# Optimization experiments

Measured on AMD Instinct MI355X. Metric: run time of the kernel, lower is better.

The kernel has to match this reference:

```python
import jax, jax.numpy as jnp
import numpy as np

N_NODES = 50000
N_EDGES = 800000
IN_FEATS = 512
NUM_HEADS = 4
OUT_FEATS = 64
NEG_SLOPE = 0.2


def setup_inputs() -> dict:
    key = jax.random.key(0)
    k1, k2, k3, k4, k5, k6 = jax.random.split(key, 6)
    feat = jax.random.normal(k1, (N_NODES, IN_FEATS), dtype=jnp.float32)
    W = jax.random.normal(k2, (IN_FEATS, NUM_HEADS * OUT_FEATS), dtype=jnp.float32) * (1.0 / np.sqrt(IN_FEATS))
    attn_l = jax.random.normal(k3, (NUM_HEADS, OUT_FEATS), dtype=jnp.float32) * (1.0 / np.sqrt(OUT_FEATS))
    attn_r = jax.random.normal(k4, (NUM_HEADS, OUT_FEATS), dtype=jnp.float32) * (1.0 / np.sqrt(OUT_FEATS))
    src = jax.random.randint(k5, (N_EDGES,), 0, N_NODES, dtype=jnp.int32)
    dst = jax.random.randint(k6, (N_EDGES,), 0, N_NODES, dtype=jnp.int32)
    return {"feat": feat, "W": W, "attn_l": attn_l, "attn_r": attn_r, "src": src, "dst": dst}


def reference(feat, W, attn_l, attn_r, src, dst):
    N = feat.shape[0]
    H, D = attn_l.shape
    # node-wise projection: fc(feat).view(N, H, D)
    ft = (feat @ W).reshape(N, H, D)
    # per-node attention logits
    el = jnp.einsum('nhd,hd->nh', ft, attn_l)  # [N, H]
    er = jnp.einsum('nhd,hd->nh', ft, attn_r)  # [N, H]
    # edge-wise score: leaky_relu(el[u] + er[v])
    e = jax.nn.leaky_relu(el[src] + er[dst], negative_slope=NEG_SLOPE)  # [E, H]
    # segment softmax over incoming edges of each destination node
    e_max = jax.ops.segment_max(e, dst, num_segments=N)  # [N, H]
    e_max = jnp.where(jnp.isfinite(e_max), e_max, 0.0)
    exp_e = jnp.exp(e - e_max[dst])  # [E, H]
    denom = jax.ops.segment_sum(exp_e, dst, num_segments=N)  # [N, H]
    a = exp_e / denom[dst]  # [E, H]
    # weighted message aggregation: sum_u a(u,v) * ft[u]
    msg = ft[src] * a[:, :, None]  # [E, H, D]
    out = jax.ops.segment_sum(msg, dst, num_segments=N)  # [N, H, D]
    return out.reshape(N, H * D)
```

## Files before the change

### kernel.cpp

```cpp
#include <hip/hip_runtime.h>

#define N_NODES 50000
#define N_EDGES 800000
#define IN_F    512
#define NH      4
#define DH      64
#define HD      256
#define NEG     0.2f
#define NB      ((N_NODES + 255) / 256)

typedef __attribute__((ext_vector_type(8))) short bf16x8;
typedef __attribute__((ext_vector_type(4))) float f32x4;

__device__ __forceinline__ unsigned short f2bf(float x) {
    unsigned u = __float_as_uint(x);
    unsigned r = (u + 0x7FFFu + ((u >> 16) & 1u)) >> 16;
    return (unsigned short)r;
}
__device__ __forceinline__ float bf2f(unsigned short b) {
    return __uint_as_float((unsigned)b << 16);
}

__global__ __launch_bounds__(256) void setup_kernel(const float* __restrict__ W,
                                                    unsigned short* __restrict__ Wtb,
                                                    int* __restrict__ counts) {
    int b = blockIdx.x;
    if (b < NB) {
        int i = b * 256 + threadIdx.x;
        if (i < N_NODES) counts[i] = 0;
    } else {
        int i = (b - NB) * 256 + threadIdx.x;
        if (i < IN_F * HD) {
            int k = i >> 8;
            int n = i & 255;
            Wtb[(size_t)n * IN_F + k] = f2bf(W[i]);
        }
    }
}

__global__ __launch_bounds__(256) void count_kernel(const int* __restrict__ dst,
                                                    int* __restrict__ counts) {
    int e = blockIdx.x * blockDim.x + threadIdx.x;
    if (e < N_EDGES) atomicAdd(&counts[dst[e]], 1);
}

#define LDPA 72
#define LDPB 72
__global__ __launch_bounds__(256) void gemm_kernel(const float* __restrict__ A,
                                                   const unsigned short* __restrict__ Wtb,
                                                   const float* __restrict__ attn_l,
                                                   const float* __restrict__ attn_r,
                                                   unsigned short* __restrict__ Cb,
                                                   float* __restrict__ el,
                                                   float* __restrict__ er) {
    __shared__ short A_s[64][LDPA];
    __shared__ short B_s[256][LDPB];

    const int tid  = threadIdx.x;
    const int lane = tid & 63;
    const int w    = tid >> 6;
    const int lm   = lane & 15;
    const int quad = lane >> 4;
    const int row0 = blockIdx.x * 64;

    const int srow = tid >> 3;
    const int sc8  = (tid & 7) * 8;

    f32x4 acc[4][4] = {};
    float4 pa[4];
    bf16x8 pb[8];

#define LOAD_TILES(KT)                                                         \
    {                                                                          \
        int g0 = row0 + srow;                                                  \
        if (g0 < N_NODES) {                                                    \
            const float* ap = A + (size_t)g0 * IN_F + (KT) + sc8;              \
            pa[0] = *(const float4*)ap; pa[1] = *(const float4*)(ap + 4);      \
        } else { pa[0] = pa[1] = make_float4(0.f, 0.f, 0.f, 0.f); }            \
        int g1 = row0 + 32 + srow;                                             \
        if (g1 < N_NODES) {                                                    \
            const float* ap = A + (size_t)g1 * IN_F + (KT) + sc8;              \
            pa[2] = *(const float4*)ap; pa[3] = *(const float4*)(ap + 4);      \
        } else { pa[2] = pa[3] = make_float4(0.f, 0.f, 0.f, 0.f); }            \
        _Pragma("unroll")                                                      \
        for (int it = 0; it < 8; it++) {                                       \
            int brow = it * 32 + srow;                                         \
            pb[it] = *(const bf16x8*)(Wtb + (size_t)brow * IN_F +              \
                                      (KT) + sc8);                             \
        }                                                                      \
    }

    LOAD_TILES(0);

    for (int kt = 0; kt < IN_F; kt += 64) {
        {
            bf16x8 s;
            s[0] = (short)f2bf(pa[0].x); s[1] = (short)f2bf(pa[0].y);
            s[2] = (short)f2bf(pa[0].z); s[3] = (short)f2bf(pa[0].w);
            s[4] = (short)f2bf(pa[1].x); s[5] = (short)f2bf(pa[1].y);
            s[6] = (short)f2bf(pa[1].z); s[7] = (short)f2bf(pa[1].w);
            *(bf16x8*)(&A_s[srow][sc8]) = s;
            s[0] = (short)f2bf(pa[2].x); s[1] = (short)f2bf(pa[2].y);
            s[2] = (short)f2bf(pa[2].z); s[3] = (short)f2bf(pa[2].w);
            s[4] = (short)f2bf(pa[3].x); s[5] = (short)f2bf(pa[3].y);
            s[6] = (short)f2bf(pa[3].z); s[7] = (short)f2bf(pa[3].w);
            *(bf16x8*)(&A_s[32 + srow][sc8]) = s;
#pragma unroll
            for (int it = 0; it < 8; it++)
                *(bf16x8*)(&B_s[it * 32 + srow][sc8]) = pb[it];
        }
        __syncthreads();

        if (kt + 64 < IN_F) LOAD_TILES(kt + 64);

#pragma unroll
        for (int kk = 0; kk < 64; kk += 32) {
            bf16x8 af[4], bfr[4];
#pragma unroll
            for (int i = 0; i < 4; i++)
                af[i] = *(const bf16x8*)(&A_s[i * 16 + lm][kk + quad * 8]);
#pragma unroll
            for (int j = 0; j < 4; j++)
                bfr[j] = *(const bf16x8*)(&B_s[w * 64 + j * 16 + lm][kk + quad * 8]);
#pragma unroll
            for (int i = 0; i < 4; i++)
#pragma unroll
                for (int j = 0; j < 4; j++)
                    acc[i][j] = __builtin_amdgcn_mfma_f32_16x16x32_bf16(
                        af[i], bfr[j], acc[i][j], 0, 0, 0);
        }
        __syncthreads();
    }
#undef LOAD_TILES

#pragma unroll
    for (int i = 0; i < 4; i++) {
#pragma unroll
        for (int j = 0; j < 4; j++) {
            int gcol = w * 64 + j * 16 + lm;
#pragma unroll
            for (int r = 0; r < 4; r++) {
                int grow = row0 + i * 16 + quad * 4 + r;
                if (grow < N_NODES)
                    Cb[(size_t)grow * HD + gcol] = f2bf(acc[i][j][r]);
            }
        }
    }

    {
        float al[4], ar[4];
#pragma unroll
        for (int j = 0; j < 4; j++) {
            al[j] = attn_l[w * DH + j * 16 + lm];
            ar[j] = attn_r[w * DH + j * 16 + lm];
        }
#pragma unroll
        for (int i = 0; i < 4; i++) {
#pragma unroll
            for (int r = 0; r < 4; r++) {
                float sl = 0.f, sr = 0.f;
#pragma unroll
                for (int j = 0; j < 4; j++) {
                    sl += acc[i][j][r] * al[j];
                    sr += acc[i][j][r] * ar[j];
                }
#pragma unroll
                for (int off = 8; off > 0; off >>= 1) {
                    sl += __shfl_xor(sl, off);
                    sr += __shfl_xor(sr, off);
                }
                if (lm == 0) {
                    int grow = row0 + i * 16 + quad * 4 + r;
                    if (grow < N_NODES) {
                        el[(size_t)grow * NH + w] = sl;
                        er[(size_t)grow * NH + w] = sr;
                    }
                }
            }
        }
    }
}

__global__ __launch_bounds__(256) void partial_kernel(const int* __restrict__ counts,
                                                      int* __restrict__ bsums) {
    __shared__ int red[4];
    int i = blockIdx.x * 256 + threadIdx.x;
    int c = (i < N_NODES) ? counts[i] : 0;
#pragma unroll
    for (int off = 32; off > 0; off >>= 1) c += __shfl_down(c, off);
    if ((threadIdx.x & 63) == 0) red[threadIdx.x >> 6] = c;
    __syncthreads();
    if (threadIdx.x == 0) bsums[blockIdx.x] = red[0] + red[1] + red[2] + red[3];
}

__global__ __launch_bounds__(256) void bscan_kernel(const int* __restrict__ bsums,
                                                    int* __restrict__ boffs) {
    __shared__ int s[256];
    int tid = threadIdx.x;
    s[tid] = (tid < NB) ? bsums[tid] : 0;
    __syncthreads();
    for (int off = 1; off < 256; off <<= 1) {
        int x = s[tid];
        int a = (tid >= off) ? s[tid - off] : 0;
        __syncthreads();
        s[tid] = x + a;
        __syncthreads();
    }
    if (tid < NB) boffs[tid] = (tid > 0) ? s[tid - 1] : 0;
}

__global__ __launch_bounds__(256) void scatter_scan_kernel(const int* __restrict__ counts,
                                                           const int* __restrict__ boffs,
                                                           int* __restrict__ offsets,
                                                           int* __restrict__ cursor) {
    __shared__ int s[256];
    int tid = threadIdx.x;
    int i = blockIdx.x * 256 + tid;
    s[tid] = (i < N_NODES) ? counts[i] : 0;
    __syncthreads();
    for (int off = 1; off < 256; off <<= 1) {
        int x = s[tid];
        int a = (tid >= off) ? s[tid - off] : 0;
        __syncthreads();
        s[tid] = x + a;
        __syncthreads();
    }
    int excl = (tid > 0) ? s[tid - 1] : 0;
    int o = boffs[blockIdx.x] + excl;
    if (i < N_NODES) { offsets[i] = o; cursor[i] = o; }
    if (i == 0) offsets[N_NODES] = N_EDGES;
}

__device__ __forceinline__ float lrelu_exp(float x) {
    float y = (x > 0.f) ? x : NEG * x;
    return __expf(y);
}

__global__ __launch_bounds__(256) void edge_place_kernel(const int* __restrict__ src,
                                                         const int* __restrict__ dst,
                                                         const float* __restrict__ el,
                                                         const float* __restrict__ er,
                                                         int* __restrict__ cursor,
                                                         int* __restrict__ srcs,
                                                         float* __restrict__ w4s) {
    int e = blockIdx.x * blockDim.x + threadIdx.x;
    if (e >= N_EDGES) return;
    int u = src[e], v = dst[e];
    float4 l = *(const float4*)(el + (size_t)u * NH);
    float4 r = *(const float4*)(er + (size_t)v * NH);
    float4 s;
    s.x = lrelu_exp(l.x + r.x);
    s.y = lrelu_exp(l.y + r.y);
    s.z = lrelu_exp(l.z + r.z);
    s.w = lrelu_exp(l.w + r.w);
    int pos = atomicAdd(&cursor[v], 1);
    srcs[pos] = u;
    *(float4*)(w4s + (size_t)pos * NH) = s;
}

__global__ __launch_bounds__(256) void agg_kernel(const unsigned short* __restrict__ ftb,
                                                  const float* __restrict__ w4s,
                                                  const int* __restrict__ srcs,
                                                  const int* __restrict__ offsets,
                                                  float* __restrict__ out) {
    int wv   = (blockIdx.x * blockDim.x + threadIdx.x) >> 6;
    int lane = threadIdx.x & 63;
    if (wv >= N_NODES) return;

    const int beg = offsets[wv];
    const int end = offsets[wv + 1];
    const int h   = lane >> 4;
    const size_t foff = (size_t)lane * 4;

    float4 acc = make_float4(0.f, 0.f, 0.f, 0.f);
    float dsum = 0.f;

    const int n4 = (end - beg) >> 2;
    int u0, u1, u2, u3;
    if (n4 > 0) {
        const int* sp = srcs + beg;
        u0 = sp[0]; u1 = sp[1]; u2 = sp[2]; u3 = sp[3];
        for (int b = 0; b < n4; b++) {
            const int base = beg + b * 4;
            int v0 = 0, v1 = 0, v2 = 0, v3 = 0;
            if (b + 1 < n4) {
                const int* np = srcs + base + 4;
                v0 = np[0]; v1 = np[1]; v2 = np[2]; v3 = np[3];
            }
            ushort4 f0 = *(const ushort4*)(ftb + (size_t)u0 * HD + foff);
            ushort4 f1 = *(const ushort4*)(ftb + (size_t)u1 * HD + foff);
            ushort4 f2 = *(const ushort4*)(ftb + (size_t)u2 * HD + foff);
            ushort4 f3 = *(const ushort4*)(ftb + (size_t)u3 * HD + foff);
            float w0 = w4s[(size_t)(base + 0) * NH + h];
            float w1 = w4s[(size_t)(base + 1) * NH + h];
            float w2 = w4s[(size_t)(base + 2) * NH + h];
            float w3 = w4s[(size_t)(base + 3) * NH + h];
            acc.x += w0 * bf2f(f0.x) + w1 * bf2f(f1.x) + w2 * bf2f(f2.x) + w3 * bf2f(f3.x);
            acc.y += w0 * bf2f(f0.y) + w1 * bf2f(f1.y) + w2 * bf2f(f2.y) + w3 * bf2f(f3.y);
            acc.z += w0 * bf2f(f0.z) + w1 * bf2f(f1.z) + w2 * bf2f(f2.z) + w3 * bf2f(f3.z);
            acc.w += w0 * bf2f(f0.w) + w1 * bf2f(f1.w) + w2 * bf2f(f2.w) + w3 * bf2f(f3.w);
            dsum += (w0 + w1) + (w2 + w3);
            u0 = v0; u1 = v1; u2 = v2; u3 = v3;
        }
    }
    for (int p = beg + n4 * 4; p < end; p++) {
        int u = srcs[p];
        float w = w4s[(size_t)p * NH + h];
        ushort4 f = *(const ushort4*)(ftb + (size_t)u * HD + foff);
        acc.x += w * bf2f(f.x);
        acc.y += w * bf2f(f.y);
        acc.z += w * bf2f(f.z);
        acc.w += w * bf2f(f.w);
        dsum += w;
    }

    float inv = (dsum > 0.f) ? (1.f / dsum) : 0.f;
    acc.x *= inv; acc.y *= inv; acc.z *= inv; acc.w *= inv;
    *(float4*)(out + (size_t)wv * HD + foff) = acc;
}

extern "C" void kernel_launch(void* const* d_in, const int* in_sizes, int n_in,
                              void* d_out, int out_size, void* d_ws, size_t ws_size,
                              hipStream_t stream) {
    const float* feat   = (const float*)d_in[0];
    const float* W      = (const float*)d_in[1];
    const float* attn_l = (const float*)d_in[2];
    const float* attn_r = (const float*)d_in[3];
    const int*   src    = (const int*)d_in[4];
    const int*   dst    = (const int*)d_in[5];
    float* out = (float*)d_out;

    char* p = (char*)d_ws;
    auto alloc = [&](size_t bytes) -> char* {
        char* r = p;
        p += (bytes + 255) & ~(size_t)255;
        return r;
    };
    unsigned short* ftb     = (unsigned short*)alloc((size_t)N_NODES * HD * 2);
    unsigned short* Wtb     = (unsigned short*)alloc((size_t)IN_F * HD * 2);
    float*          el      = (float*)alloc((size_t)N_NODES * NH * 4);
    float*          er      = (float*)alloc((size_t)N_NODES * NH * 4);
    float*          w4s     = (float*)alloc((size_t)N_EDGES * NH * 4);
    int*            srcs    = (int*)alloc((size_t)N_EDGES * 4);
    int*            counts  = (int*)alloc((size_t)N_NODES * 4);
    int*            offsets = (int*)alloc((size_t)(N_NODES + 1) * 4);
    int*            cursor  = (int*)alloc((size_t)N_NODES * 4);
    int*            bsums   = (int*)alloc((size_t)NB * 4);
    int*            boffs   = (int*)alloc((size_t)NB * 4);

    setup_kernel<<<NB + (IN_F * HD + 255) / 256, 256, 0, stream>>>(W, Wtb, counts);
    count_kernel<<<(N_EDGES + 255) / 256, 256, 0, stream>>>(dst, counts);
    gemm_kernel<<<(N_NODES + 63) / 64, 256, 0, stream>>>(feat, Wtb, attn_l, attn_r,
                                                         ftb, el, er);
    partial_kernel<<<NB, 256, 0, stream>>>(counts, bsums);
    bscan_kernel<<<1, 256, 0, stream>>>(bsums, boffs);
    scatter_scan_kernel<<<NB, 256, 0, stream>>>(counts, boffs, offsets, cursor);
    edge_place_kernel<<<(N_EDGES + 255) / 256, 256, 0, stream>>>(src, dst, el, er,
                                                                 cursor, srcs, w4s);
    agg_kernel<<<(N_NODES + 3) / 4, 256, 0, stream>>>(ftb, w4s, srcs, offsets, out);
}
```

Before: 345.0 us.

## Fuse edge weights into aggregation, stage W via direct-to-LDS double-buffered loads

Edge attention weights are no longer computed and written in edge_place_kernel. agg_kernel now recomputes leaky_relu+exp from el[src] and er[dst], which removes the w4s buffer (write plus read of 12.8MB). The aggregation loop is unrolled to 8 edges, with a masked branchless tail. The GEMM pre-swizzles W into tiled XOR-permuted blocks and streams them with global_load_lds into a double-buffered LDS tile, dropping register staging for B. In exchange, LDS use goes up to 64KB for B, and el is gathered redundantly per edge.

Result: no change. 345.6 us (+0.2%).

```diff
diff --git a/kernel.cpp b/kernel.cpp
--- a/kernel.cpp
+++ b/kernel.cpp
@@ -22,7 +22,7 @@
 }
 
 __global__ __launch_bounds__(256) void setup_kernel(const float* __restrict__ W,
-                                                    unsigned short* __restrict__ Wtb,
+                                                    unsigned short* __restrict__ WtbT,
                                                     int* __restrict__ counts) {
     int b = blockIdx.x;
     if (b < NB) {
@@ -33,7 +33,12 @@
         if (i < IN_F * HD) {
             int k = i >> 8;
             int n = i & 255;
-            Wtb[(size_t)n * IN_F + k] = f2bf(W[i]);
+            int t  = k >> 6;
+            int kk = k & 63;
+            int g  = kk >> 3;
+            int w8 = kk & 7;
+            int p  = n * 8 + (g ^ (n & 7));
+            WtbT[(size_t)t * 16384 + p * 8 + w8] = f2bf(W[i]);
         }
     }
 }
@@ -45,16 +50,15 @@
 }
 
 #define LDPA 72
-#define LDPB 72
 __global__ __launch_bounds__(256) void gemm_kernel(const float* __restrict__ A,
-                                                   const unsigned short* __restrict__ Wtb,
+                                                   const unsigned short* __restrict__ WtbT,
                                                    const float* __restrict__ attn_l,
                                                    const float* __restrict__ attn_r,
                                                    unsigned short* __restrict__ Cb,
                                                    float* __restrict__ el,
                                                    float* __restrict__ er) {
     __shared__ short A_s[64][LDPA];
-    __shared__ short B_s[256][LDPB];
+    __shared__ short B_s[2][256 * 64];
 
     const int tid  = threadIdx.x;
     const int lane = tid & 63;
@@ -68,9 +72,20 @@
 
     f32x4 acc[4][4] = {};
     float4 pa[4];
-    bf16x8 pb[8];
-
-#define LOAD_TILES(KT)                                                         \
+
+#define STAGE_B(BUF, T)                                                         \
+    {                                                                           \
+        const char* gsrc = (const char*)WtbT + (size_t)(T) * 32768 + tid * 16;  \
+        char* ldst = (char*)&B_s[BUF][0] + tid * 16;                            \
+        _Pragma("unroll")                                                       \
+        for (int r = 0; r < 8; r++)                                             \
+            __builtin_amdgcn_global_load_lds(                                   \
+                (const __attribute__((address_space(1))) unsigned int*)(gsrc + r * 4096), \
+                (__attribute__((address_space(3))) unsigned int*)(ldst + r * 4096),       \
+                16, 0, 0);                                                      \
+    }
+
+#define LOAD_A(KT)                                                             \
     {                                                                          \
         int g0 = row0 + srow;                                                  \
         if (g0 < N_NODES) {                                                    \
@@ -82,17 +97,13 @@
             const float* ap = A + (size_t)g1 * IN_F + (KT) + sc8;              \
             pa[2] = *(const float4*)ap; pa[3] = *(const float4*)(ap + 4);      \
         } else { pa[2] = pa[3] = make_float4(0.f, 0.f, 0.f, 0.f); }            \
-        _Pragma("unroll")                                                      \
-        for (int it = 0; it < 8; it++) {                                       \
-            int brow = it * 32 + srow;                                         \
-            pb[it] = *(const bf16x8*)(Wtb + (size_t)brow * IN_F +              \
-                                      (KT) + sc8);                             \
-        }                                                                      \
-    }
-
-    LOAD_TILES(0);
-
-    for (int kt = 0; kt < IN_F; kt += 64) {
+    }
+
+    STAGE_B(0, 0);
+    LOAD_A(0);
+
+    int buf = 0;
+    for (int t = 0; t < 8; t++) {
         {
             bf16x8 s;
             s[0] = (short)f2bf(pa[0].x); s[1] = (short)f2bf(pa[0].y);
@@ -105,13 +116,10 @@
             s[4] = (short)f2bf(pa[3].x); s[5] = (short)f2bf(pa[3].y);
             s[6] = (short)f2bf(pa[3].z); s[7] = (short)f2bf(pa[3].w);
             *(bf16x8*)(&A_s[32 + srow][sc8]) = s;
-#pragma unroll
-            for (int it = 0; it < 8; it++)
-                *(bf16x8*)(&B_s[it * 32 + srow][sc8]) = pb[it];
         }
         __syncthreads();
 
-        if (kt + 64 < IN_F) LOAD_TILES(kt + 64);
+        if (t + 1 < 8) { STAGE_B(buf ^ 1, t + 1); LOAD_A((t + 1) * 64); }
 
 #pragma unroll
         for (int kk = 0; kk < 64; kk += 32) {
@@ -120,8 +128,12 @@
             for (int i = 0; i < 4; i++)
                 af[i] = *(const bf16x8*)(&A_s[i * 16 + lm][kk + quad * 8]);
 #pragma unroll
-            for (int j = 0; j < 4; j++)
-                bfr[j] = *(const bf16x8*)(&B_s[w * 64 + j * 16 + lm][kk + quad * 8]);
+            for (int j = 0; j < 4; j++) {
+                int n  = w * 64 + j * 16 + lm;
+                int g  = (kk >> 3) + quad;
+                int gs = g ^ (lm & 7);
+                bfr[j] = *(const bf16x8*)(&B_s[buf][(n * 8 + gs) * 8]);
+            }
 #pragma unroll
             for (int i = 0; i < 4; i++)
 #pragma unroll
@@ -129,9 +141,11 @@
                     acc[i][j] = __builtin_amdgcn_mfma_f32_16x16x32_bf16(
                         af[i], bfr[j], acc[i][j], 0, 0, 0);
         }
-        __syncthreads();
-    }
-#undef LOAD_TILES
+        if (t < 7) __syncthreads();
+        buf ^= 1;
+    }
+#undef LOAD_A
+#undef STAGE_B
 
 #pragma unroll
     for (int i = 0; i < 4; i++) {
@@ -231,35 +245,25 @@
     if (i == 0) offsets[N_NODES] = N_EDGES;
 }
 
-__device__ __forceinline__ float lrelu_exp(float x) {
-    float y = (x > 0.f) ? x : NEG * x;
-    return __expf(y);
-}
-
 __global__ __launch_bounds__(256) void edge_place_kernel(const int* __restrict__ src,
                                                          const int* __restrict__ dst,
-                                                         const float* __restrict__ el,
-                                                         const float* __restrict__ er,
                                                          int* __restrict__ cursor,
-                                                         int* __restrict__ srcs,
-                                                         float* __restrict__ w4s) {
+                                                         int* __restrict__ srcs) {
     int e = blockIdx.x * blockDim.x + threadIdx.x;
     if (e >= N_EDGES) return;
     int u = src[e], v = dst[e];
-    float4 l = *(const float4*)(el + (size_t)u * NH);
-    float4 r = *(const float4*)(er + (size_t)v * NH);
-    float4 s;
-    s.x = lrelu_exp(l.x + r.x);
-    s.y = lrelu_exp(l.y + r.y);
-    s.z = lrelu_exp(l.z + r.z);
-    s.w = lrelu_exp(l.w + r.w);
     int pos = atomicAdd(&cursor[v], 1);
     srcs[pos] = u;
-    *(float4*)(w4s + (size_t)pos * NH) = s;
+}
+
+__device__ __forceinline__ float lrelu_exp(float x) {
+    float y = fmaxf(x, NEG * x);
+    return __expf(y);
 }
 
 __global__ __launch_bounds__(256) void agg_kernel(const unsigned short* __restrict__ ftb,
-                                                  const float* __restrict__ w4s,
+                                                  const float* __restrict__ el,
+                                                  const float* __restrict__ er,
                                                   const int* __restrict__ srcs,
                                                   const int* __restrict__ offsets,
                                                   float* __restrict__ out) {
@@ -271,47 +275,101 @@
     const int end = offsets[wv + 1];
     const int h   = lane >> 4;
     const size_t foff = (size_t)lane * 4;
+    const float erv = er[(size_t)wv * NH + h];
 
     float4 acc = make_float4(0.f, 0.f, 0.f, 0.f);
     float dsum = 0.f;
 
-    const int n4 = (end - beg) >> 2;
-    int u0, u1, u2, u3;
-    if (n4 > 0) {
+    const int n8 = (end - beg) >> 3;
+    int u0, u1, u2, u3, u4, u5, u6, u7;
+    if (n8 > 0) {
         const int* sp = srcs + beg;
         u0 = sp[0]; u1 = sp[1]; u2 = sp[2]; u3 = sp[3];
-        for (int b = 0; b < n4; b++) {
-            const int base = beg + b * 4;
-            int v0 = 0, v1 = 0, v2 = 0, v3 = 0;
-            if (b + 1 < n4) {
-                const int* np = srcs + base + 4;
+        u4 = sp[4]; u5 = sp[5]; u6 = sp[6]; u7 = sp[7];
+        for (int b = 0; b < n8; b++) {
+            const int base = beg + b * 8;
+            int v0 = 0, v1 = 0, v2 = 0, v3 = 0, v4 = 0, v5 = 0, v6 = 0, v7 = 0;
+            if (b + 1 < n8) {
+                const int* np = srcs + base + 8;
                 v0 = np[0]; v1 = np[1]; v2 = np[2]; v3 = np[3];
+                v4 = np[4]; v5 = np[5]; v6 = np[6]; v7 = np[7];
             }
             ushort4 f0 = *(const ushort4*)(ftb + (size_t)u0 * HD + foff);
             ushort4 f1 = *(const ushort4*)(ftb + (size_t)u1 * HD + foff);
             ushort4 f2 = *(const ushort4*)(ftb + (size_t)u2 * HD + foff);
             ushort4 f3 = *(const ushort4*)(ftb + (size_t)u3 * HD + foff);
-            float w0 = w4s[(size_t)(base + 0) * NH + h];
-            float w1 = w4s[(size_t)(base + 1) * NH + h];
-            float w2 = w4s[(size_t)(base + 2) * NH + h];
-            float w3 = w4s[(size_t)(base + 3) * NH + h];
-            acc.x += w0 * bf2f(f0.x) + w1 * bf2f(f1.x) + w2 * bf2f(f2.x) + w3 * bf2f(f3.x);
-            acc.y += w0 * bf2f(f0.y) + w1 * bf2f(f1.y) + w2 * bf2f(f2.y) + w3 * bf2f(f3.y);
-            acc.z += w0 * bf2f(f0.z) + w1 * bf2f(f1.z) + w2 * bf2f(f2.z) + w3 * bf2f(f3.z);
-            acc.w += w0 * bf2f(f0.w) + w1 * bf2f(f1.w) + w2 * bf2f(f2.w) + w3 * bf2f(f3.w);
-            dsum += (w0 + w1) + (w2 + w3);
+            ushort4 f4 = *(const ushort4*)(ftb + (size_t)u4 * HD + foff);
+            ushort4 f5 = *(const ushort4*)(ftb + (size_t)u5 * HD + foff);
+            ushort4 f6 = *(const ushort4*)(ftb + (size_t)u6 * HD + foff);
+            ushort4 f7 = *(const ushort4*)(ftb + (size_t)u7 * HD + foff);
+            float e0 = el[(size_t)u0 * NH + h];
+            float e1 = el[(size_t)u1 * NH + h];
+            float e2 = el[(size_t)u2 * NH + h];
+            float e3 = el[(size_t)u3 * NH + h];
+            float e4 = el[(size_t)u4 * NH + h];
+            float e5 = el[(size_t)u5 * NH + h];
+            float e6 = el[(size_t)u6 * NH + h];
+            float e7 = el[(size_t)u7 * NH + h];
+            float w0 = lrelu_exp(e0 + erv), w1 = lrelu_exp(e1 + erv);
+            float w2 = lrelu_exp(e2 + erv), w3 = lrelu_exp(e3 + erv);
+            float w4 = lrelu_exp(e4 + erv), w5 = lrelu_exp(e5 + erv);
+            float w6 = lrelu_exp(e6 + erv), w7 = lrelu_exp(e7 + erv);
+            acc.x += w0 * bf2f(f0.x) + w1 * bf2f(f1.x) + w2 * bf2f(f2.x) + w3 * bf2f(f3.x)
+                   + w4 * bf2f(f4.x) + w5 * bf2f(f5.x) + w6 * bf2f(f6.x) + w7 * bf2f(f7.x);
+            acc.y += w0 * bf2f(f0.y) + w1 * bf2f(f1.y) + w2 * bf2f(f2.y) + w3 * bf2f(f3.y)
+                   + w4 * bf2f(f4.y) + w5 * bf2f(f5.y) + w6 * bf2f(f6.y) + w7 * bf2f(f7.y);
+            acc.z += w0 * bf2f(f0.z) + w1 * bf2f(f1.z) + w2 * bf2f(f2.z) + w3 * bf2f(f3.z)
+                   + w4 * bf2f(f4.z) + w5 * bf2f(f5.z) + w6 * bf2f(f6.z) + w7 * bf2f(f7.z);
+            acc.w += w0 * bf2f(f0.w) + w1 * bf2f(f1.w) + w2 * bf2f(f2.w) + w3 * bf2f(f3.w)
+                   + w4 * bf2f(f4.w) + w5 * bf2f(f5.w) + w6 * bf2f(f6.w) + w7 * bf2f(f7.w);
+            dsum += ((w0 + w1) + (w2 + w3)) + ((w4 + w5) + (w6 + w7));
             u0 = v0; u1 = v1; u2 = v2; u3 = v3;
-        }
-    }
-    for (int p = beg + n4 * 4; p < end; p++) {
-        int u = srcs[p];
-        float w = w4s[(size_t)p * NH + h];
-        ushort4 f = *(const ushort4*)(ftb + (size_t)u * HD + foff);
-        acc.x += w * bf2f(f.x);
-        acc.y += w * bf2f(f.y);
-        acc.z += w * bf2f(f.z);
-        acc.w += w * bf2f(f.w);
-        dsum += w;
+            u4 = v4; u5 = v5; u6 = v6; u7 = v7;
+        }
+    }
+    {
+        const int p0  = beg + n8 * 8;
+        const int rem = end - p0;
+        if (rem > 0) {
+            const int* sp = srcs + p0;
+            int x0 = sp[0];
+            int x1 = (1 < rem) ? sp[1] : x0;
+            int x2 = (2 < rem) ? sp[2] : x0;
+            int x3 = (3 < rem) ? sp[3] : x0;
+            int x4 = (4 < rem) ? sp[4] : x0;
+            int x5 = (5 < rem) ? sp[5] : x0;
+            int x6 = (6 < rem) ? sp[6] : x0;
+            ushort4 f0 = *(const ushort4*)(ftb + (size_t)x0 * HD + foff);
+            ushort4 f1 = *(const ushort4*)(ftb + (size_t)x1 * HD + foff);
+            ushort4 f2 = *(const ushort4*)(ftb + (size_t)x2 * HD + foff);
+            ushort4 f3 = *(const ushort4*)(ftb + (size_t)x3 * HD + foff);
+            ushort4 f4 = *(const ushort4*)(ftb + (size_t)x4 * HD + foff);
+            ushort4 f5 = *(const ushort4*)(ftb + (size_t)x5 * HD + foff);
+            ushort4 f6 = *(const ushort4*)(ftb + (size_t)x6 * HD + foff);
+            float e0 = el[(size_t)x0 * NH + h];
+            float e1 = el[(size_t)x1 * NH + h];
+            float e2 = el[(size_t)x2 * NH + h];
+            float e3 = el[(size_t)x3 * NH + h];
+            float e4 = el[(size_t)x4 * NH + h];
+            float e5 = el[(size_t)x5 * NH + h];
+            float e6 = el[(size_t)x6 * NH + h];
+            float w0 = lrelu_exp(e0 + erv);
+            float w1 = (1 < rem) ? lrelu_exp(e1 + erv) : 0.f;
+            float w2 = (2 < rem) ? lrelu_exp(e2 + erv) : 0.f;
+            float w3 = (3 < rem) ? lrelu_exp(e3 + erv) : 0.f;
+            float w4 = (4 < rem) ? lrelu_exp(e4 + erv) : 0.f;
+            float w5 = (5 < rem) ? lrelu_exp(e5 + erv) : 0.f;
+            float w6 = (6 < rem) ? lrelu_exp(e6 + erv) : 0.f;
+            acc.x += w0 * bf2f(f0.x) + w1 * bf2f(f1.x) + w2 * bf2f(f2.x) + w3 * bf2f(f3.x)
+                   + w4 * bf2f(f4.x) + w5 * bf2f(f5.x) + w6 * bf2f(f6.x);
+            acc.y += w0 * bf2f(f0.y) + w1 * bf2f(f1.y) + w2 * bf2f(f2.y) + w3 * bf2f(f3.y)
+                   + w4 * bf2f(f4.y) + w5 * bf2f(f5.y) + w6 * bf2f(f6.y);
+            acc.z += w0 * bf2f(f0.z) + w1 * bf2f(f1.z) + w2 * bf2f(f2.z) + w3 * bf2f(f3.z)
+                   + w4 * bf2f(f4.z) + w5 * bf2f(f5.z) + w6 * bf2f(f6.z);
+            acc.w += w0 * bf2f(f0.w) + w1 * bf2f(f1.w) + w2 * bf2f(f2.w) + w3 * bf2f(f3.w)
+                   + w4 * bf2f(f4.w) + w5 * bf2f(f5.w) + w6 * bf2f(f6.w);
+            dsum += ((w0 + w1) + (w2 + w3)) + ((w4 + w5) + w6);
+        }
     }
 
     float inv = (dsum > 0.f) ? (1.f / dsum) : 0.f;
@@ -337,10 +395,9 @@
         return r;
     };
     unsigned short* ftb     = (unsigned short*)alloc((size_t)N_NODES * HD * 2);
-    unsigned short* Wtb     = (unsigned short*)alloc((size_t)IN_F * HD * 2);
+    unsigned short* WtbT    = (unsigned short*)alloc((size_t)IN_F * HD * 2);
     float*          el      = (float*)alloc((size_t)N_NODES * NH * 4);
     float*          er      = (float*)alloc((size_t)N_NODES * NH * 4);
-    float*          w4s     = (float*)alloc((size_t)N_EDGES * NH * 4);
     int*            srcs    = (int*)alloc((size_t)N_EDGES * 4);
     int*            counts  = (int*)alloc((size_t)N_NODES * 4);
     int*            offsets = (int*)alloc((size_t)(N_NODES + 1) * 4);
@@ -348,14 +405,13 @@
     int*            bsums   = (int*)alloc((size_t)NB * 4);
     int*            boffs   = (int*)alloc((size_t)NB * 4);
 
-    setup_kernel<<<NB + (IN_F * HD + 255) / 256, 256, 0, stream>>>(W, Wtb, counts);
+    setup_kernel<<<NB + (IN_F * HD + 255) / 256, 256, 0, stream>>>(W, WtbT, counts);
     count_kernel<<<(N_EDGES + 255) / 256, 256, 0, stream>>>(dst, counts);
-    gemm_kernel<<<(N_NODES + 63) / 64, 256, 0, stream>>>(feat, Wtb, attn_l, attn_r,
+    gemm_kernel<<<(N_NODES + 63) / 64, 256, 0, stream>>>(feat, WtbT, attn_l, attn_r,
                                                          ftb, el, er);
     partial_kernel<<<NB, 256, 0, stream>>>(counts, bsums);
     bscan_kernel<<<1, 256, 0, stream>>>(bsums, boffs);
     scatter_scan_kernel<<<NB, 256, 0, stream>>>(counts, boffs, offsets, cursor);
-    edge_place_kernel<<<(N_EDGES + 255) / 256, 256, 0, stream>>>(src, dst, el, er,
-                                                                 cursor, srcs, w4s);
-    agg_kernel<<<(N_NODES + 3) / 4, 256, 0, stream>>>(ftb, w4s, srcs, offsets, out);
-}
+    edge_place_kernel<<<(N_EDGES + 255) / 256, 256, 0, stream>>>(src, dst, cursor, srcs);
+    agg_kernel<<<(N_NODES + 3) / 4, 256, 0, stream>>>(ftb, el, er, srcs, offsets, out);
+}
```
